# Kernel tuning notes

Hardware: AMD Instinct MI355X
Metric: run time of the kernel (lower is better)

## Reference

```python
import math
from collections import deque
import jax, jax.numpy as jnp
import numpy as np

PS = 16; DF = 256; DS = 16; DLANG = 896; BETA = 2.0
B_SZ = 2; IMG = 512


def setup_inputs():
    key = jax.random.key(0)
    ks = jax.random.split(key, 16)
    def rn(k, shape, scale=1.0):
        return jax.random.normal(k, shape, jnp.float32) * scale
    # W_delta bias init: inverse-softplus of dt ~ LogUniform(1e-3, 1e-1), as in torch _init_weights
    u = jax.random.uniform(ks[15], (DF,), jnp.float32)
    dt = jnp.exp(u * (math.log(0.1) - math.log(0.001)) + math.log(0.001))
    inv_dt = dt + jnp.log(-jnp.expm1(-dt))
    return {
        "images": rn(ks[0], (B_SZ, 3, IMG, IMG)),
        "lang_g": rn(ks[1], (B_SZ, DLANG)),
        "conv1_w": rn(ks[2], (64, 3, 3, 3), 1.0 / math.sqrt(27)),
        "conv1_b": jnp.zeros((64,), jnp.float32),
        "conv2_w": rn(ks[3], (128, 64, 3, 3), 1.0 / math.sqrt(576)),
        "conv2_b": jnp.zeros((128,), jnp.float32),
        "fc_w": rn(ks[4], (DF, 128), 1.0 / math.sqrt(128)),
        "fc_b": jnp.zeros((DF,), jnp.float32),
        "W_gate": rn(ks[5], (DF, DLANG), 1.0 / math.sqrt(DLANG)),
        "W_g_prime": rn(ks[6], (DF, DLANG), 1.0 / math.sqrt(DLANG)),
        "A_log": jnp.log(jnp.broadcast_to(jnp.arange(1, DS + 1, dtype=jnp.float32), (DF, DS))),
        "D": jnp.ones((DF,), jnp.float32),
        "B_w": rn(ks[7], (DS, DF), 1.0 / math.sqrt(DF)),
        "B_b": jnp.zeros((DS,), jnp.float32),
        "C_w": rn(ks[8], (DS, DF), 1.0 / math.sqrt(DF)),
        "C_b": jnp.zeros((DS,), jnp.float32),
        "Wd_w": rn(ks[9], (DF, DF), 1.0 / math.sqrt(DF)),
        "Wd_b": inv_dt,
        "out_w": rn(ks[10], (DF, DF), 1.0 / math.sqrt(DF)),
        "out_b": jnp.zeros((DF,), jnp.float32),
        "ln_g": jnp.ones((DF,), jnp.float32),
        "ln_b": jnp.zeros((DF,), jnp.float32),
    }


def _gelu(x):
    return jax.nn.gelu(x, approximate=False)  # torch nn.GELU() default = exact erf


def _conv(x, w, b):
    y = jax.lax.conv_general_dilated(x, w, (1, 1), 'SAME', dimension_numbers=('NCHW', 'OIHW', 'NCHW'))
    return y + b[None, :, None, None]


def _patch_feats(images, c1w, c1b, c2w, c2b, fcw, fcb):
    B, C, H, W = images.shape
    nH, nW = H // PS, W // PS
    # non-overlapping patchify (== unfold/unfold in torch)
    p = images.reshape(B, C, nH, PS, nW, PS).transpose(0, 2, 4, 1, 3, 5).reshape(B * nH * nW, C, PS, PS)
    h = _gelu(_conv(p, c1w, c1b))
    h = _gelu(_conv(h, c2w, c2b))
    h = h.mean(axis=(2, 3))  # AdaptiveAvgPool2d((1,1))
    feats = (h @ fcw.T + fcb).reshape(B, nH * nW, DF)
    return feats, nH, nW


def _structure(feats, r_sem, nH, nW):
    # Host-side (numpy) Kruskal MST + BFS ordering, mirroring the torch detach().cpu() path.
    f = np.asarray(feats, np.float32)
    r = np.asarray(r_sem, np.float32)
    B, P, _ = f.shape
    src, dst = [], []
    for i in range(nH):
        for j in range(nW):
            u = i * nW + j
            if j + 1 < nW:
                src.append(u); dst.append(u + 1)
            if i + 1 < nH:
                src.append(u); dst.append(u + nW)
    src = np.array(src); dst = np.array(dst)
    bfs_all, par_all = [], []
    for b in range(B):
        fn = f[b] / np.maximum(np.linalg.norm(f[b], axis=1, keepdims=True), 1e-12)
        cos = (fn[src] * fn[dst]).sum(1)
        w = (1.0 - r[b][src]) * (1.0 - r[b][dst]) * (-cos) + 1e-6
        parent = np.arange(P)
        def find(x):
            while parent[x] != x:
                parent[x] = parent[parent[x]]
                x = parent[x]
            return x
        adj = [[] for _ in range(P)]
        cnt = 0
        for idx in np.argsort(w):
            ru, rv = find(int(src[idx])), find(int(dst[idx]))
            if ru != rv:
                parent[ru] = rv
                adj[src[idx]].append(int(dst[idx]))
                adj[dst[idx]].append(int(src[idx]))
                cnt += 1
                if cnt == P - 1:
                    break
        root = int(r[b].argmax())
        vis = [False] * P; par_of = [-1] * P; bfs = []
        q = deque([root]); vis[root] = True
        while q:
            n = q.popleft()
            bfs.append(n)
            for nb in adj[n]:
                if not vis[nb]:
                    vis[nb] = True
                    par_of[nb] = n
                    q.append(nb)
        o2b = [0] * P
        for bi, oi in enumerate(bfs):
            o2b[oi] = bi
        par_bfs = [-1 if par_of[o] == -1 else o2b[par_of[o]] for o in bfs]
        bfs_all.append(bfs); par_all.append(par_bfs)
    return jnp.array(bfs_all, jnp.int32), jnp.array(par_all, jnp.int32)


def _core(feats, r_sem, g_prime, bfs, par, A_log, D, B_w, B_b, C_w, C_b, Wd_w, Wd_b, out_w, out_b, ln_g, ln_b):
    A = -jnp.exp(A_log)  # (DF, DS)
    def one(f_b, r_b, gp, bfs_b, par_b):
        rs = r_b[bfs_b]                                  # (P,)
        X = f_b[bfs_b] + rs[:, None] * gp[None, :]       # (P, DF)
        delta = jax.nn.softplus(X @ Wd_w.T + Wd_b) * (1.0 + BETA * rs[:, None])
        Bp = X @ B_w.T + B_b                             # (P, DS)
        Cp = X @ C_w.T + C_b                             # (P, DS)
        P = X.shape[0]
        def body(H, inp):
            i, d_i, b_i, c_i, x_i, p_i = inp
            A_bar = jnp.exp(d_i[:, None] * A)            # (DF, DS)
            h_par = H[jnp.maximum(p_i, 0)] * (p_i >= 0)  # zeros at root
            h = A_bar * h_par + (d_i[:, None] * b_i[None, :]) * x_i[:, None]
            H = H.at[i].set(h)
            y = (h * c_i[None, :]).sum(-1) + D * x_i
            return H, y
        H0 = jnp.zeros((P, DF, DS), X.dtype)
        _, Y = jax.lax.scan(body, H0, (jnp.arange(P), delta, Bp, Cp, X, par_b))
        Yr = jnp.zeros_like(Y).at[bfs_b].set(Y)          # scatter back to raster order
        o = Yr @ out_w.T + out_b
        mu = o.mean(-1, keepdims=True)
        v = ((o - mu) ** 2).mean(-1, keepdims=True)
        return ln_g * (o - mu) / jnp.sqrt(v + 1e-5) + ln_b
    return jax.vmap(one)(feats, r_sem, g_prime, bfs, par)


def reference(images, lang_g, conv1_w, conv1_b, conv2_w, conv2_b, fc_w, fc_b, W_gate, W_g_prime, A_log, D, B_w, B_b, C_w, C_b, Wd_w, Wd_b, out_w, out_b, ln_g, ln_b):
    feats, nH, nW = _patch_feats(images, conv1_w, conv1_b, conv2_w, conv2_b, fc_w, fc_b)
    g_proj = lang_g @ W_gate.T
    r_sem = jax.nn.sigmoid(jnp.einsum('bd,bpd->bp', g_proj, feats) / math.sqrt(DF))
    bfs, par = _structure(feats, r_sem, nH, nW)
    g_prime = lang_g @ W_g_prime.T
    return _core(feats, r_sem, g_prime, bfs, par, A_log, D, B_w, B_b, C_w, C_b, Wd_w, Wd_b, out_w, out_b, ln_g, ln_b)
```

## Files before the change

### kernel.cpp

```cpp
#include <hip/hip_runtime.h>
#include <cstddef>
#include <cstdint>

#define NB    2
#define NP    1024
#define DFEAT 256
#define DSTATE 16
#define NEDGE 1984

typedef unsigned short ushortb;

typedef float fx16 __attribute__((ext_vector_type(16)));
typedef short s16x8 __attribute__((ext_vector_type(8)));

__device__ __forceinline__ float bf2f(unsigned short u){
  union { unsigned int i; float f; } c; c.i = ((unsigned int)u) << 16; return c.f;
}
__device__ __forceinline__ unsigned short f2bf(float f){
  union { float f; unsigned int i; } c; c.f = f;
  unsigned int u = c.i;
  unsigned int r = (u + 0x7fffu + ((u >> 16) & 1u)) >> 16;
  return (unsigned short)r;
}
__device__ __forceinline__ float ldin(const void* p, size_t i, int isbf){
  return isbf ? bf2f(((const ushortb*)p)[i]) : ((const float*)p)[i];
}
__device__ __forceinline__ float gelu_f(float x){
  return 0.5f * x * (1.0f + erff(x * 0.70710678118654752f));
}
__device__ __forceinline__ unsigned int f2sort(float f){
  union { float f; unsigned int i; } c; c.f = f;
  return (c.i & 0x80000000u) ? ~c.i : (c.i | 0x80000000u);
}

constexpr size_t AL(size_t x){ return (x + 63) & ~(size_t)63; }
constexpr size_t O_W1    = 0;
constexpr size_t O_B1    = AL(O_W1 + 1728);
constexpr size_t O_W2    = AL(O_B1 + 64);
constexpr size_t O_B2    = AL(O_W2 + 73728);
constexpr size_t O_FCW   = AL(O_B2 + 128);
constexpr size_t O_FCB   = AL(O_FCW + 32768);
constexpr size_t O_WDW   = AL(O_FCB + 256);
constexpr size_t O_WDB   = AL(O_WDW + 65536);
constexpr size_t O_BWO   = AL(O_WDB + 256);
constexpr size_t O_BBO   = AL(O_BWO + 4096);
constexpr size_t O_CWO   = AL(O_BBO + 16);
constexpr size_t O_CBO   = AL(O_CWO + 4096);
constexpr size_t O_OW    = AL(O_CBO + 16);
constexpr size_t O_OB    = AL(O_OW + 65536);
constexpr size_t O_AF    = AL(O_OB + 256);
constexpr size_t O_DD    = AL(O_AF + 4096);
constexpr size_t O_LNG   = AL(O_DD + 256);
constexpr size_t O_LNB   = AL(O_LNG + 256);
constexpr size_t O_FEATS = AL(O_LNB + 256);
constexpr size_t O_GPROJ = AL(O_FEATS + (size_t)NB*NP*DFEAT);
constexpr size_t O_GPRIM = AL(O_GPROJ + NB*DFEAT);
constexpr size_t O_RSEM  = AL(O_GPRIM + NB*DFEAT);
constexpr size_t O_BFS   = AL(O_RSEM + NB*NP);
constexpr size_t O_PAR   = AL(O_BFS + NB*NP);
constexpr size_t O_X     = AL(O_PAR + NB*NP);
constexpr size_t O_DELTA = AL(O_X + (size_t)NB*NP*DFEAT);
constexpr size_t O_BP    = AL(O_DELTA + (size_t)NB*NP*DFEAT);
constexpr size_t O_CP    = AL(O_BP + NB*NP*DSTATE);
constexpr size_t O_YR    = AL(O_CP + NB*NP*DSTATE);
constexpr size_t O_FLAG  = AL(O_YR + (size_t)NB*NP*DFEAT);
constexpr size_t O_LVL   = AL(O_FLAG + 64);

__global__ __launch_bounds__(256) void k_sniff(const void* img, float* ws)
{
  __shared__ int cnt;
  int tid = threadIdx.x;
  if (tid == 0) cnt = 0;
  __syncthreads();
  const ushortb* u = (const ushortb*)img;
  int local = 0;
  for (int k = 0; k < 16; k++){
    unsigned short v = u[tid * 16 + k];
    if (v == 0 || v == 0x8000u){ local++; continue; }
    float f = fabsf(bf2f(v));
    if (f >= 1e-8f && f <= 64.f) local++;
  }
  atomicAdd(&cnt, local);
  __syncthreads();
  if (tid == 0) ((int*)(ws + O_FLAG))[0] = (cnt >= 3900) ? 1 : 0;
}

__global__ __launch_bounds__(256) void k_convert(const void* c1w, const void* c1b, const void* c2w,
                          const void* c2b, const void* fcw, const void* fcb,
                          const void* alog, const void* dvec,
                          const void* bw, const void* bb, const void* cw, const void* cb,
                          const void* wdw, const void* wdb,
                          const void* ow, const void* ob,
                          const void* lng, const void* lnb,
                          const void* lang, const void* wgate, const void* wgp,
                          float* ws)
{
  const int F = ((const int*)(ws + O_FLAG))[0];
  if (blockIdx.x >= 3038){
    int row = (blockIdx.x - 3038) * 4 + (threadIdx.x >> 6);
    int lane = threadIdx.x & 63;
    int mat = row >> 9;
    int b   = (row >> 8) & 1;
    int df  = row & 255;
    const void* W = mat ? wgp : wgate;
    float s = 0.f;
    for (int k = lane; k < 896; k += 64)
      s += ldin(lang, (size_t)b * 896 + k, F) * ldin(W, (size_t)df * 896 + k, F);
    s += __shfl_xor(s, 1);  s += __shfl_xor(s, 2);  s += __shfl_xor(s, 4);
    s += __shfl_xor(s, 8);  s += __shfl_xor(s, 16); s += __shfl_xor(s, 32);
    if (lane == 0) ws[(mat ? O_GPRIM : O_GPROJ) + b * 256 + df] = s;
    return;
  }
  if (blockIdx.x >= 990){
    size_t i2 = (size_t)(blockIdx.x - 990) * 256 + threadIdx.x;
    if (i2 < (size_t)NB * NP * DFEAT) ws[O_YR + i2] = 0.f;
    return;
  }
  int i = blockIdx.x * 256 + threadIdx.x;
  if (i < 1728){ ws[O_W1 + i] = ldin(c1w, i, F); return; } i -= 1728;
  if (i < 64){ ws[O_B1 + i] = ldin(c1b, i, F); return; } i -= 64;
  if (i < 73728){
    int sg = i >> 11;
    int r = i & 2047;
    int nt = r >> 9;
    int r2 = r & 511;
    int ln = r2 >> 3, e = r2 & 7;
    int c  = sg / 18, s = sg - c * 18;
    int tap = s >> 1, ksub = s & 1;
    int oc = nt * 32 + (ln & 31);
    int ic = c * 32 + ksub * 16 + (ln >> 5) * 8 + e;
    float v = ldin(c2w, (size_t)(oc * 64 + ic) * 9 + tap, F);
    ushortb hi = f2bf(v);
    float lo = v - bf2f(hi);
    ushortb* WB = (ushortb*)(ws + O_W2);
    size_t cb = ((size_t)(sg * 4 + nt)) * 2;
    WB[cb * 512 + r2]       = hi;
    WB[(cb + 1) * 512 + r2] = f2bf(lo);
    return;
  } i -= 73728;
  if (i < 128){ ws[O_B2 + i] = ldin(c2b, i, F); return; } i -= 128;
  if (i < 32768){ ws[O_FCW + i] = ldin(fcw, i, F); return; } i -= 32768;
  if (i < 256){ ws[O_FCB + i] = ldin(fcb, i, F); return; } i -= 256;
  if (i < 65536){
    int k = i >> 8, df = i & 255;
    ws[O_WDW + i] = ldin(wdw, (size_t)df * 256 + k, F); return;
  } i -= 65536;
  if (i < 256){ ws[O_WDB + i] = ldin(wdb, i, F); return; } i -= 256;
  if (i < 4096){
    int k = i >> 4, s = i & 15;
    ws[O_BWO + i] = ldin(bw, (size_t)s * 256 + k, F); return;
  } i -= 4096;
  if (i < 16){ ws[O_BBO + i] = ldin(bb, i, F); return; } i -= 16;
  if (i < 4096){
    int k = i >> 4, s = i & 15;
    ws[O_CWO + i] = ldin(cw, (size_t)s * 256 + k, F); return;
  } i -= 4096;
  if (i < 16){ ws[O_CBO + i] = ldin(cb, i, F); return; } i -= 16;
  if (i < 65536){
    int k = i >> 8, df = i & 255;
    ws[O_OW + i] = ldin(ow, (size_t)df * 256 + k, F); return;
  } i -= 65536;
  if (i < 256){ ws[O_OB + i] = ldin(ob, i, F); return; } i -= 256;
  if (i < 4096){ ws[O_AF + i] = -expf(ldin(alog, i, F)); return; } i -= 4096;
  if (i < 256){ ws[O_DD + i] = ldin(dvec, i, F); return; } i -= 256;
  if (i < 256){ ws[O_LNG + i] = ldin(lng, i, F); return; } i -= 256;
  if (i < 256){ ws[O_LNB + i] = ldin(lnb, i, F); }
}

__global__ __launch_bounds__(512, 4) void k_patch(const void* __restrict__ img,
                                                  const float* __restrict__ ws,
                                                  float* __restrict__ feats)
{
  __shared__ __align__(16) ushortb Abuf[2 * 10368];
  __shared__ float timg[768];
  __shared__ float pool4[512];
  __shared__ float pm[128];
  const int F = ((const int*)(ws + O_FLAG))[0];
  const float* W1 = ws + O_W1;  const float* B1 = ws + O_B1;
  const float* FCW = ws + O_FCW; const float* FCB = ws + O_FCB;
  const s16x8* BF = (const s16x8*)(ws + O_W2);

  int blk = blockIdx.x; int b = blk >> 10; int pidx = blk & 1023;
  int ph = pidx >> 5, pw = pidx & 31;
  int tid = threadIdx.x;

  if (tid < 256){
    int y = tid >> 4, x = tid & 15;
    #pragma unroll
    for (int c = 0; c < 3; c++)
      timg[c * 256 + tid] =
        ldin(img, (((size_t)b * 3 + c) * 512 + (ph * 16 + y)) * 512 + (pw * 16 + x), F);
  }
  {
    uint4 z4 = make_uint4(0u, 0u, 0u, 0u);
    for (int r = tid; r < 324; r += 512){
      int y = r / 18, x = r - y * 18;
      if (y == 0 || y == 17 || x == 0 || x == 17){
        #pragma unroll
        for (int m = 0; m < 4; m++){
          *(uint4*)&Abuf[r * 32 + m * 8] = z4;
          *(uint4*)&Abuf[10368 + r * 32 + m * 8] = z4;
        }
      }
    }
  }
  __syncthreads();

  int wv = tid >> 6, ln = tid & 63;
  int mg = wv >> 1, ng = wv & 1;
  int l31 = ln & 31, lhi = ln >> 5;
  int xcol = ln & 15, yrow = l31 >> 4;
  int p = tid & 255, og = tid >> 8;
  int ii = p >> 4, jj = p & 15;

  fx16 acc00, acc01, acc10, acc11;
  #pragma unroll
  for (int r = 0; r < 16; r++){ acc00[r] = 0.f; acc01[r] = 0.f; acc10[r] = 0.f; acc11[r] = 0.f; }

  for (int c = 0; c < 2; c++){
    {
      float pin[27];
      #pragma unroll
      for (int cc = 0; cc < 3; cc++)
        #pragma unroll
        for (int dy = 0; dy < 3; dy++)
          #pragma unroll
          for (int dx = 0; dx < 3; dx++){
            int y = ii + dy - 1, x = jj + dx - 1;
            bool ok = (y >= 0 && y < 16 && x >= 0 && x < 16);
            pin[cc * 9 + dy * 3 + dx] = ok ? timg[cc * 256 + y * 16 + x] : 0.f;
          }
      int oc0 = c * 32 + og * 16;
      int w1base = __builtin_amdgcn_readfirstlane(oc0 * 27);
      const float* W1g = W1 + w1base;
      int r = (ii + 1) * 18 + (jj + 1);
      int swz = ((r >> 1) & 3) << 3;
      #pragma unroll
      for (int g = 0; g < 2; g++){
        float av[8];
        #pragma unroll
        for (int o = 0; o < 8; o++){
          float a = B1[oc0 + g * 8 + o];
          #pragma unroll
          for (int t = 0; t < 27; t++) a += W1g[(g * 8 + o) * 27 + t] * pin[t];
          av[o] = gelu_f(a);
        }
        unsigned int hp[4], lp[4];
        #pragma unroll
        for (int q = 0; q < 4; q++){
          float v0 = av[2 * q], v1 = av[2 * q + 1];
          ushortb h0 = f2bf(v0), h1 = f2bf(v1);
          float l0 = v0 - bf2f(h0), l1 = v1 - bf2f(h1);
          hp[q] = (unsigned int)h0 | ((unsigned int)h1 << 16);
          lp[q] = (unsigned int)f2bf(l0) | ((unsigned int)f2bf(l1) << 16);
        }
        int idx = r * 32 + (((og * 2 + g) << 3) ^ swz);
        *(uint4*)&Abuf[idx] = make_uint4(hp[0], hp[1], hp[2], hp[3]);
        *(uint4*)&Abuf[10368 + idx] = make_uint4(lp[0], lp[1], lp[2], lp[3]);
      }
    }
    __syncthreads();

    {
      const s16x8* bfp = BF + (size_t)((c * 144 + ng * 4) * 64 + ln);
      for (int s = 0; s < 18; s++){
        int tap = s >> 1, ksub = s & 1;
        int dyq = tap / 3, dxq = tap - dyq * 3;
        int icq0 = (ksub << 1) + lhi;
        int rA = (mg * 4 + yrow + dyq) * 18 + (xcol + dxq);
        int rB = rA + 36;
        int iA0 = rA * 32 + ((icq0 ^ ((rA >> 1) & 3)) << 3);
        int iA1 = rB * 32 + ((icq0 ^ ((rB >> 1) & 3)) << 3);
        s16x8 fa0h = *(const s16x8*)&Abuf[iA0];
        s16x8 fa0l = *(const s16x8*)&Abuf[10368 + iA0];
        s16x8 fa1h = *(const s16x8*)&Abuf[iA1];
        s16x8 fa1l = *(const s16x8*)&Abuf[10368 + iA1];
        const s16x8* bq = bfp + (s << 9);
        s16x8 fb0h = bq[0];
        s16x8 fb0l = bq[64];
        s16x8 fb1h = bq[128];
        s16x8 fb1l = bq[192];
        acc00 = __builtin_amdgcn_mfma_f32_32x32x16_bf16(fa0h, fb0h, acc00, 0, 0, 0);
        acc01 = __builtin_amdgcn_mfma_f32_32x32x16_bf16(fa0h, fb1h, acc01, 0, 0, 0);
        acc10 = __builtin_amdgcn_mfma_f32_32x32x16_bf16(fa1h, fb0h, acc10, 0, 0, 0);
        acc11 = __builtin_amdgcn_mfma_f32_32x32x16_bf16(fa1h, fb1h, acc11, 0, 0, 0);
        acc00 = __builtin_amdgcn_mfma_f32_32x32x16_bf16(fa0l, fb0h, acc00, 0, 0, 0);
        acc01 = __builtin_amdgcn_mfma_f32_32x32x16_bf16(fa0l, fb1h, acc01, 0, 0, 0);
        acc10 = __builtin_amdgcn_mfma_f32_32x32x16_bf16(fa1l, fb0h, acc10, 0, 0, 0);
        acc11 = __builtin_amdgcn_mfma_f32_32x32x16_bf16(fa1l, fb1h, acc11, 0, 0, 0);
        acc00 = __builtin_amdgcn_mfma_f32_32x32x16_bf16(fa0h, fb0l, acc00, 0, 0, 0);
        acc01 = __builtin_amdgcn_mfma_f32_32x32x16_bf16(fa0h, fb1l, acc01, 0, 0, 0);
        acc10 = __builtin_amdgcn_mfma_f32_32x32x16_bf16(fa1h, fb0l, acc10, 0, 0, 0);
        acc11 = __builtin_amdgcn_mfma_f32_32x32x16_bf16(fa1h, fb1l, acc11, 0, 0, 0);
      }
    }
    __syncthreads();
  }

  #pragma unroll
  for (int n = 0; n < 2; n++){
    int nt = ng * 2 + n;
    float bz = ws[O_B2 + nt * 32 + l31];
    float sum = 0.f;
    #pragma unroll
    for (int r = 0; r < 16; r++)
      sum += gelu_f(((n == 0) ? acc00[r] : acc01[r]) + bz)
           + gelu_f(((n == 0) ? acc10[r] : acc11[r]) + bz);
    sum += __shfl_xor(sum, 32);
    if (lhi == 0) pool4[mg * 128 + nt * 32 + l31] = sum;
  }
  __syncthreads();
  if (tid < 128){
    float sv = pool4[tid] + pool4[128 + tid] + pool4[256 + tid] + pool4[384 + tid];
    pm[tid] = sv * (1.f / 256.f);
  }
  __syncthreads();

  if (tid < 256){
    int df = tid;
    float s = FCB[df];
    const float* wrow = FCW + (size_t)df * 128;
    #pragma unroll
    for (int k = 0; k < 128; k += 4)
      s += wrow[k] * pm[k] + wrow[k + 1] * pm[k + 1]
         + wrow[k + 2] * pm[k + 2] + wrow[k + 3] * pm[k + 3];
    feats[((size_t)(b * 1024 + pidx)) * 256 + df] = s;
  }
}

__device__ __forceinline__ void edge_uv(int e, int& u, int& v){
  if (e < 1953){
    int i = e / 63; int k = e - i * 63;
    if (k < 62){ int j = k >> 1; u = i * 32 + j; v = (k & 1) ? u + 32 : u + 1; }
    else { u = i * 32 + 31; v = u + 32; }
  } else { u = 31 * 32 + (e - 1953); v = u + 1; }
}

__global__ __launch_bounds__(1024) void k_struct(float* __restrict__ ws)
{
  __shared__ float s_ninv[1024];
  __shared__ float s_w[NEDGE];
  __shared__ float s_r[1024];
  __shared__ int   s_comp[1024];
  __shared__ int   s_link[1024];
  __shared__ int   s_link2[1024];
  __shared__ unsigned long long s_best[1024];
  __shared__ unsigned char  s_mst[NEDGE];
  __shared__ unsigned short s_adj[1024 * 4];
  __shared__ unsigned char  s_deg[1024];
  __shared__ unsigned short s_bfs[1024];
  __shared__ short          s_parof[1024];
  __shared__ unsigned short s_o2b[1024];
  __shared__ unsigned short s_cur[1024];
  __shared__ unsigned short s_nxt[1024];
  __shared__ unsigned short s_off[1025];
  __shared__ unsigned short s_loff2[1026];
  __shared__ unsigned long long s_rootkey;
  __shared__ int s_ncomp, s_cursz, s_bfscnt, s_nextsz, s_nlvl;

  int b = blockIdx.x; int tid = threadIdx.x;
  const float* feats = ws + O_FEATS + (size_t)b * NP * DFEAT;

  {
    const float4* f4 = (const float4*)(feats + (size_t)tid * 256);
    const float4* g4 = (const float4*)(ws + O_GPROJ + b * 256);
    float d = 0.f, gdot = 0.f;
    for (int k = 0; k < 64; k++){
      float4 q = f4[k]; float4 g = g4[k];
      d += q.x*q.x + q.y*q.y + q.z*q.z + q.w*q.w;
      gdot += q.x*g.x + q.y*g.y + q.z*g.z + q.w*g.w;
    }
    s_ninv[tid] = 1.f / fmaxf(sqrtf(d), 1e-12f);
    float r = 1.f / (1.f + expf(-gdot * (1.f / 16.f)));
    s_r[tid] = r;
    ws[O_RSEM + b * NP + tid] = r;
    s_comp[tid] = tid;
    s_deg[tid] = 0;
    s_bfs[tid] = (unsigned short)tid;
    s_o2b[tid] = (unsigned short)tid;
    s_parof[tid] = -1;
  }
  for (int e = tid; e < NEDGE; e += 1024) s_mst[e] = 0;
  __syncthreads();

  for (int e = tid; e < NEDGE; e += 1024){
    int u, v; edge_uv(e, u, v);
    const float4* fu = (const float4*)(feats + (size_t)u * 256);
    const float4* fv = (const float4*)(feats + (size_t)v * 256);
    float d = 0.f;
    for (int k = 0; k < 64; k++){ float4 a = fu[k], c = fv[k]; d += a.x*c.x + a.y*c.y + a.z*c.z + a.w*c.w; }
    float cosv = d * s_ninv[u] * s_ninv[v];
    s_w[e] = (1.f - s_r[u]) * (1.f - s_r[v]) * (-cosv) + 1e-6f;
  }
  __syncthreads();

  for (int round = 0; round < 12; round++){
    s_best[tid] = ~0ull;
    __syncthreads();
    for (int e = tid; e < NEDGE; e += 1024){
      int u, v; edge_uv(e, u, v);
      int cu = s_comp[u], cv = s_comp[v];
      if (cu != cv){
        unsigned long long key = (((unsigned long long)f2sort(s_w[e])) << 32) | (unsigned int)e;
        atomicMin(&s_best[cu], key);
        atomicMin(&s_best[cv], key);
      }
    }
    __syncthreads();
    int l = tid;
    if (s_comp[tid] == tid && s_best[tid] != ~0ull){
      int e = (int)(s_best[tid] & 0xffffffffu);
      int u, v; edge_uv(e, u, v);
      s_mst[e] = 1;
      int cu = s_comp[u], cv = s_comp[v];
      l = (cu == tid) ? cv : cu;
    }
    s_link[tid] = l;
    __syncthreads();
    if (l != tid && s_link[l] == tid && tid < l) s_link[tid] = tid;
    __syncthreads();
    {
      int x = tid;
      int p = s_link[x];
      while (p != x){ x = p; p = s_link[x]; }
      s_link2[tid] = x;
    }
    __syncthreads();
    s_comp[tid] = s_link2[s_comp[tid]];
    if (tid == 0) s_ncomp = 0;
    __syncthreads();
    if (s_comp[tid] == tid) atomicAdd(&s_ncomp, 1);
    __syncthreads();
    if (s_ncomp == 1) break;
    __syncthreads();
  }
  __syncthreads();

  {
    int v = tid; int i = v >> 5, j = v & 31;
    float wloc[4]; int nloc[4]; int d = 0;
    if (j > 0){ int e = (i < 31) ? (i * 63 + 2 * (j - 1)) : (1953 + (j - 1));
      if (s_mst[e]){ wloc[d] = s_w[e]; nloc[d] = v - 1; d++; } }
    if (j < 31){ int e = (i < 31) ? (i * 63 + 2 * j) : (1953 + j);
      if (s_mst[e]){ wloc[d] = s_w[e]; nloc[d] = v + 1; d++; } }
    if (i > 0){ int e = (i - 1) * 63 + ((j < 31) ? (2 * j + 1) : 62);
      if (s_mst[e]){ wloc[d] = s_w[e]; nloc[d] = v - 32; d++; } }
    if (i < 31){ int e = i * 63 + ((j < 31) ? (2 * j + 1) : 62);
      if (s_mst[e]){ wloc[d] = s_w[e]; nloc[d] = v + 32; d++; } }
    for (int a = 1; a < d; a++){
      float wv = wloc[a]; int nv = nloc[a]; int c = a - 1;
      while (c >= 0 && wloc[c] > wv){ wloc[c+1] = wloc[c]; nloc[c+1] = nloc[c]; c--; }
      wloc[c+1] = wv; nloc[c+1] = nv;
    }
    s_deg[v] = (unsigned char)d;
    for (int a = 0; a < d; a++) s_adj[v * 4 + a] = (unsigned short)nloc[a];
  }
  if (tid == 0) s_rootkey = 0ull;
  __syncthreads();
  {
    unsigned long long key = (((unsigned long long)f2sort(s_r[tid])) << 32) | (unsigned int)(1023 - tid);
    atomicMax(&s_rootkey, key);
  }
  __syncthreads();
  int root = 1023 - (int)(s_rootkey & 0xffffffffu);

  if (tid == 0){
    s_bfs[0] = (unsigned short)root; s_o2b[root] = 0; s_parof[root] = -1;
    s_cur[0] = (unsigned short)root; s_cursz = 1; s_bfscnt = 1; s_nlvl = 0;
  }
  __syncthreads();
  for (int lev = 0; lev < 1024; lev++){
    int csz = s_cursz;
    if (csz <= 0) break;
    if (tid < 64){
      int runbase = 0;
      for (int t0 = 0; t0 < csz; t0 += 64){
        int t = t0 + tid;
        int cnt = 0;
        if (t < csz){
          int n = s_cur[t];
          cnt = (int)s_deg[n] - (s_parof[n] >= 0 ? 1 : 0);
        }
        int v = cnt;
        #pragma unroll
        for (int off = 1; off < 64; off <<= 1){
          int u2 = __shfl_up(v, off);
          if (tid >= off) v += u2;
        }
        if (t < csz) s_off[t] = (unsigned short)(runbase + v - cnt);
        runbase += __shfl(v, 63);
      }
      if (tid == 0){
        if (s_nlvl < 1025){ s_loff2[s_nlvl] = (unsigned short)(s_bfscnt - csz); }
        s_nlvl++;
        s_nextsz = runbase;
      }
    }
    __syncthreads();
    if (tid < csz){
      int n = s_cur[tid]; int base = s_off[tid]; int k = 0;
      int pn = s_parof[n]; int dg = s_deg[n];
      for (int a = 0; a < dg; a++){
        int c = s_adj[n * 4 + a];
        if (c == pn) continue;
        s_parof[c] = (short)n;
        if (base + k < 1024) s_nxt[base + k] = (unsigned short)c;
        int pos = s_bfscnt + base + k;
        if (pos < 1024){
          s_bfs[pos] = (unsigned short)c;
          s_o2b[c] = (unsigned short)pos;
        }
        k++;
      }
    }
    __syncthreads();
    if (tid == 0){ s_bfscnt += s_nextsz; s_cursz = (s_nextsz > 1024) ? 1024 : s_nextsz; }
    __syncthreads();
    if (tid < s_cursz) s_cur[tid] = s_nxt[tid];
    __syncthreads();
  }
  __syncthreads();

  int* BFSo = (int*)(ws + O_BFS);
  int* PARo = (int*)(ws + O_PAR);
  {
    int node = s_bfs[tid] & 1023;
    BFSo[b * 1024 + tid] = node;
    int p = s_parof[node];
    PARo[b * 1024 + tid] = (p < 0) ? -1 : (int)(s_o2b[p] & 1023);
  }
  {
    int* LVLo = (int*)(ws + O_LVL) + b * 1040;
    int nl = s_nlvl; if (nl > 1024) nl = 1024;
    if (tid == 0){ LVLo[0] = nl; LVLo[1 + nl] = NP; }
    if (tid < nl) LVLo[1 + tid] = (int)s_loff2[tid];
  }
}

__global__ __launch_bounds__(256) void k_xdelta(float* __restrict__ ws)
{
  __shared__ float xs[256];
  int blk = blockIdx.x; int b = blk >> 10, i = blk & 1023; int df = threadIdx.x;
  const int* BFSo = (const int*)(ws + O_BFS);
  int node = BFSo[b * 1024 + i] & 1023;
  float rs = ws[O_RSEM + b * 1024 + node];
  float xv = ws[O_FEATS + ((size_t)(b * 1024 + node)) * 256 + df] + rs * ws[O_GPRIM + b * 256 + df];
  xs[df] = xv;
  ws[O_X + ((size_t)(b * 1024 + i)) * 256 + df] = xv;
  __syncthreads();
  {
    const float* WT = ws + O_WDW;
    float z = ws[O_WDB + df];
    #pragma unroll 8
    for (int k = 0; k < 256; k++)
      z += WT[(size_t)k * 256 + df] * xs[k];
    float sp = fmaxf(z, 0.f) + log1pf(expf(-fabsf(z)));
    ws[O_DELTA + ((size_t)(b * 1024 + i)) * 256 + df] = sp * (1.f + 2.f * rs);
  }
  if (df < 32){
    int s = df & 15;
    const float* WT = ws + ((df < 16) ? O_BWO : O_CWO);
    float a = ws[((df < 16) ? O_BBO : O_CBO) + s];
    #pragma unroll 8
    for (int k = 0; k < 256; k++) a += WT[k * 16 + s] * xs[k];
    ws[((df < 16) ? O_BP : O_CP) + (size_t)(b * 1024 + i) * 16 + s] = a;
  }
}

__global__ __launch_bounds__(256) void k_scan(float* __restrict__ ws)
{
  __shared__ float h[NP * DSTATE];
  __shared__ float xs[NP];
  __shared__ float ds[NP];
  __shared__ int   par_s[NP];
  __shared__ int   bfs_s[NP];
  int blk = blockIdx.x; int b = blk >> 8, f = blk & 255;
  int tid = threadIdx.x;
  int g = tid >> 4, s = tid & 15;
  const int* PARo = (const int*)(ws + O_PAR);
  const int* BFSo = (const int*)(ws + O_BFS);
  const int* LVLo = (const int*)(ws + O_LVL) + b * 1040;
  for (int i = tid; i < NP; i += 256){
    xs[i] = ws[O_X     + ((size_t)(b * NP + i)) * DFEAT + f];
    ds[i] = ws[O_DELTA + ((size_t)(b * NP + i)) * DFEAT + f];
    par_s[i] = PARo[b * NP + i];
    bfs_s[i] = BFSo[b * NP + i] & 1023;
  }
  __syncthreads();

  int nlvl = LVLo[0];
  bool degen = (nlvl < 1 || nlvl > NP);
  if (degen) nlvl = NP;

  float Aln = ws[O_AF + f * 16 + s];
  float Dv  = ws[O_DD + f];
  const float* Bp = ws + O_BP + (size_t)b * NP * DSTATE;
  const float* Cp = ws + O_CP + (size_t)b * NP * DSTATE;
  float* Yr = ws + O_YR + (size_t)b * NP * DFEAT;

  for (int l = 0; l < nlvl; l++){
    int o0, o1;
    if (degen){ o0 = l; o1 = l + 1; }
    else {
      o0 = LVLo[1 + l]; o1 = LVLo[2 + l];
      o0 = (o0 < 0) ? 0 : ((o0 > NP) ? NP : o0);
      o1 = (o1 < o0) ? o0 : ((o1 > NP) ? NP : o1);
    }
    for (int i = o0 + g; i < o1; i += 16){
      int p = par_s[i];
      float d = ds[i], x = xs[i];
      float hp = (p >= 0 && p < i) ? h[p * 16 + s] : 0.f;
      float hn = expf(d * Aln) * hp + d * Bp[i * 16 + s] * x;
      h[i * 16 + s] = hn;
      float t = hn * Cp[i * 16 + s];
      t += __shfl_xor(t, 1); t += __shfl_xor(t, 2);
      t += __shfl_xor(t, 4); t += __shfl_xor(t, 8);
      if (s == 0) Yr[(size_t)bfs_s[i] * DFEAT + f] = t + Dv * x;
    }
    __syncthreads();
  }
}

__global__ __launch_bounds__(256) void k_outln(const float* __restrict__ ws,
                                               void* __restrict__ out)
{
  __shared__ float yl[256];
  __shared__ float red[8];
  const int F = ((const int*)(ws + O_FLAG))[0];
  int blk = blockIdx.x; int b = blk >> 10, p = blk & 1023; int df = threadIdx.x;
  yl[df] = ws[O_YR + ((size_t)(b * 1024 + p)) * 256 + df];
  __syncthreads();
  const float* OT = ws + O_OW;
  float a = ws[O_OB + df];
  #pragma unroll 8
  for (int k = 0; k < 256; k++)
    a += OT[(size_t)k * 256 + df] * yl[k];
  int lane = df & 63, wid = df >> 6;
  float t = a;
  t += __shfl_xor(t, 1); t += __shfl_xor(t, 2);  t += __shfl_xor(t, 4);
  t += __shfl_xor(t, 8); t += __shfl_xor(t, 16); t += __shfl_xor(t, 32);
  if (lane == 0) red[wid] = t;
  __syncthreads();
  float mu = (red[0] + red[1] + red[2] + red[3]) * (1.f / 256.f);
  float dv = a - mu;
  float t2 = dv * dv;
  t2 += __shfl_xor(t2, 1); t2 += __shfl_xor(t2, 2);  t2 += __shfl_xor(t2, 4);
  t2 += __shfl_xor(t2, 8); t2 += __shfl_xor(t2, 16); t2 += __shfl_xor(t2, 32);
  if (lane == 0) red[4 + wid] = t2;
  __syncthreads();
  float var = (red[4] + red[5] + red[6] + red[7]) * (1.f / 256.f);
  float o = ws[O_LNG + df] * dv / sqrtf(var + 1e-5f) + ws[O_LNB + df];
  size_t idx = ((size_t)(b * 1024 + p)) * 256 + df;
  if (F) ((ushortb*)out)[idx] = f2bf(o);
  else   ((float*)out)[idx]   = o;
}

extern "C" void kernel_launch(void* const* d_in, const int* in_sizes, int n_in,
                              void* d_out, int out_size, void* d_ws, size_t ws_size,
                              hipStream_t stream)
{
  (void)in_sizes; (void)n_in; (void)out_size; (void)ws_size;
  const void* img   = d_in[0];
  const void* lang  = d_in[1];
  const void* c1w   = d_in[2];
  const void* c1b   = d_in[3];
  const void* c2w   = d_in[4];
  const void* c2b   = d_in[5];
  const void* fcw   = d_in[6];
  const void* fcb   = d_in[7];
  const void* wgate = d_in[8];
  const void* wgp   = d_in[9];
  const void* alog  = d_in[10];
  const void* dvec  = d_in[11];
  const void* bw    = d_in[12];
  const void* bb    = d_in[13];
  const void* cw    = d_in[14];
  const void* cb    = d_in[15];
  const void* wdw   = d_in[16];
  const void* wdb   = d_in[17];
  const void* ow    = d_in[18];
  const void* ob    = d_in[19];
  const void* lng   = d_in[20];
  const void* lnb   = d_in[21];
  float* ws = (float*)d_ws;

  k_sniff<<<1, 256, 0, stream>>>(img, ws);
  k_convert<<<990 + 2048 + 256, 256, 0, stream>>>(c1w, c1b, c2w, c2b, fcw, fcb, alog, dvec,
                                                  bw, bb, cw, cb, wdw, wdb, ow, ob, lng, lnb,
                                                  lang, wgate, wgp, ws);
  k_patch<<<2048, 512, 0, stream>>>(img, ws, ws + O_FEATS);
  k_struct<<<2, 1024, 0, stream>>>(ws);
  k_xdelta<<<2048, 256, 0, stream>>>(ws);
  k_scan<<<NB * DFEAT, 256, 0, stream>>>(ws);
  k_outln<<<2048, 256, 0, stream>>>(ws, d_out);
}
```

Before: 886.0 us.

## Stage both conv1 channel halves in LDS and split conv2 MFMA by row per wave

The conv1 output for both 32-channel halves is now computed once into a doubled LDS buffer, which removes the mid-loop barriers and the second pass. Conv2 tiling changes so that each of the 8 waves owns two output rows and loops over two output-channel passes with two accumulators, instead of a 2x4 mg/ng split with four accumulators. This cuts register pressure and barriers, but doubles the LDS footprint (about 83KB), which may lower occupancy, and each wave now reloads the B fragments for every pass.

```diff
diff --git a/kernel.cpp b/kernel.cpp
--- a/kernel.cpp
+++ b/kernel.cpp
@@ -171,9 +171,9 @@
                                                   const float* __restrict__ ws,
                                                   float* __restrict__ feats)
 {
-  __shared__ __align__(16) ushortb Abuf[2 * 10368];
+  __shared__ __align__(16) ushortb Abuf[4 * 10368];
   __shared__ float timg[768];
-  __shared__ float pool4[512];
+  __shared__ float pool8[8 * 128];
   __shared__ float pm[128];
   const int F = ((const int*)(ws + O_FLAG))[0];
   const float* W1 = ws + O_W1;  const float* B1 = ws + O_B1;
@@ -197,44 +197,39 @@
       int y = r / 18, x = r - y * 18;
       if (y == 0 || y == 17 || x == 0 || x == 17){
         #pragma unroll
-        for (int m = 0; m < 4; m++){
-          *(uint4*)&Abuf[r * 32 + m * 8] = z4;
-          *(uint4*)&Abuf[10368 + r * 32 + m * 8] = z4;
-        }
+        for (int pl = 0; pl < 4; pl++)
+          #pragma unroll
+          for (int m = 0; m < 4; m++)
+            *(uint4*)&Abuf[pl * 10368 + r * 32 + m * 8] = z4;
       }
     }
   }
   __syncthreads();
 
   int wv = tid >> 6, ln = tid & 63;
-  int mg = wv >> 1, ng = wv & 1;
   int l31 = ln & 31, lhi = ln >> 5;
   int xcol = ln & 15, yrow = l31 >> 4;
   int p = tid & 255, og = tid >> 8;
   int ii = p >> 4, jj = p & 15;
 
-  fx16 acc00, acc01, acc10, acc11;
-  #pragma unroll
-  for (int r = 0; r < 16; r++){ acc00[r] = 0.f; acc01[r] = 0.f; acc10[r] = 0.f; acc11[r] = 0.f; }
-
-  for (int c = 0; c < 2; c++){
-    {
-      float pin[27];
+  {
+    float pin[27];
+    #pragma unroll
+    for (int cc = 0; cc < 3; cc++)
       #pragma unroll
-      for (int cc = 0; cc < 3; cc++)
+      for (int dy = 0; dy < 3; dy++)
         #pragma unroll
-        for (int dy = 0; dy < 3; dy++)
-          #pragma unroll
-          for (int dx = 0; dx < 3; dx++){
-            int y = ii + dy - 1, x = jj + dx - 1;
-            bool ok = (y >= 0 && y < 16 && x >= 0 && x < 16);
-            pin[cc * 9 + dy * 3 + dx] = ok ? timg[cc * 256 + y * 16 + x] : 0.f;
-          }
+        for (int dx = 0; dx < 3; dx++){
+          int y = ii + dy - 1, x = jj + dx - 1;
+          bool ok = (y >= 0 && y < 16 && x >= 0 && x < 16);
+          pin[cc * 9 + dy * 3 + dx] = ok ? timg[cc * 256 + y * 16 + x] : 0.f;
+        }
+    int r = (ii + 1) * 18 + (jj + 1);
+    int swz = ((r >> 1) & 3) << 3;
+    for (int c = 0; c < 2; c++){
       int oc0 = c * 32 + og * 16;
       int w1base = __builtin_amdgcn_readfirstlane(oc0 * 27);
       const float* W1g = W1 + w1base;
-      int r = (ii + 1) * 18 + (jj + 1);
-      int swz = ((r >> 1) & 3) << 3;
       #pragma unroll
       for (int g = 0; g < 2; g++){
         float av[8];
@@ -255,63 +250,61 @@
           lp[q] = (unsigned int)f2bf(l0) | ((unsigned int)f2bf(l1) << 16);
         }
         int idx = r * 32 + (((og * 2 + g) << 3) ^ swz);
-        *(uint4*)&Abuf[idx] = make_uint4(hp[0], hp[1], hp[2], hp[3]);
-        *(uint4*)&Abuf[10368 + idx] = make_uint4(lp[0], lp[1], lp[2], lp[3]);
+        *(uint4*)&Abuf[c * 20736 + idx] = make_uint4(hp[0], hp[1], hp[2], hp[3]);
+        *(uint4*)&Abuf[c * 20736 + 10368 + idx] = make_uint4(lp[0], lp[1], lp[2], lp[3]);
       }
     }
-    __syncthreads();
-
-    {
-      const s16x8* bfp = BF + (size_t)((c * 144 + ng * 4) * 64 + ln);
+  }
+  __syncthreads();
+
+  #pragma unroll
+  for (int pass = 0; pass < 2; pass++){
+    fx16 acc0, acc1;
+    #pragma unroll
+    for (int r = 0; r < 16; r++){ acc0[r] = 0.f; acc1[r] = 0.f; }
+
+    for (int c = 0; c < 2; c++){
+      const ushortb* Ah = Abuf + c * 20736;
+      const s16x8* bfp = BF + (size_t)((c * 144 + pass * 4) * 64 + ln);
       for (int s = 0; s < 18; s++){
         int tap = s >> 1, ksub = s & 1;
         int dyq = tap / 3, dxq = tap - dyq * 3;
         int icq0 = (ksub << 1) + lhi;
-        int rA = (mg * 4 + yrow + dyq) * 18 + (xcol + dxq);
-        int rB = rA + 36;
-        int iA0 = rA * 32 + ((icq0 ^ ((rA >> 1) & 3)) << 3);
-        int iA1 = rB * 32 + ((icq0 ^ ((rB >> 1) & 3)) << 3);
-        s16x8 fa0h = *(const s16x8*)&Abuf[iA0];
-        s16x8 fa0l = *(const s16x8*)&Abuf[10368 + iA0];
-        s16x8 fa1h = *(const s16x8*)&Abuf[iA1];
-        s16x8 fa1l = *(const s16x8*)&Abuf[10368 + iA1];
+        int rA = (wv * 2 + yrow + dyq) * 18 + (xcol + dxq);
+        int iA = rA * 32 + ((icq0 ^ ((rA >> 1) & 3)) << 3);
+        s16x8 fa_h = *(const s16x8*)&Ah[iA];
+        s16x8 fa_l = *(const s16x8*)&Ah[10368 + iA];
         const s16x8* bq = bfp + (s << 9);
         s16x8 fb0h = bq[0];
         s16x8 fb0l = bq[64];
         s16x8 fb1h = bq[128];
         s16x8 fb1l = bq[192];
-        acc00 = __builtin_amdgcn_mfma_f32_32x32x16_bf16(fa0h, fb0h, acc00, 0, 0, 0);
-        acc01 = __builtin_amdgcn_mfma_f32_32x32x16_bf16(fa0h, fb1h, acc01, 0, 0, 0);
-        acc10 = __builtin_amdgcn_mfma_f32_32x32x16_bf16(fa1h, fb0h, acc10, 0, 0, 0);
-        acc11 = __builtin_amdgcn_mfma_f32_32x32x16_bf16(fa1h, fb1h, acc11, 0, 0, 0);
-        acc00 = __builtin_amdgcn_mfma_f32_32x32x16_bf16(fa0l, fb0h, acc00, 0, 0, 0);
-        acc01 = __builtin_amdgcn_mfma_f32_32x32x16_bf16(fa0l, fb1h, acc01, 0, 0, 0);
-        acc10 = __builtin_amdgcn_mfma_f32_32x32x16_bf16(fa1l, fb0h, acc10, 0, 0, 0);
-        acc11 = __builtin_amdgcn_mfma_f32_32x32x16_bf16(fa1l, fb1h, acc11, 0, 0, 0);
-        acc00 = __builtin_amdgcn_mfma_f32_32x32x16_bf16(fa0h, fb0l, acc00, 0, 0, 0);
-        acc01 = __builtin_amdgcn_mfma_f32_32x32x16_bf16(fa0h, fb1l, acc01, 0, 0, 0);
-        acc10 = __builtin_amdgcn_mfma_f32_32x32x16_bf16(fa1h, fb0l, acc10, 0, 0, 0);
-        acc11 = __builtin_amdgcn_mfma_f32_32x32x16_bf16(fa1h, fb1l, acc11, 0, 0, 0);
+        acc0 = __builtin_amdgcn_mfma_f32_32x32x16_bf16(fa_h, fb0h, acc0, 0, 0, 0);
+        acc1 = __builtin_amdgcn_mfma_f32_32x32x16_bf16(fa_h, fb1h, acc1, 0, 0, 0);
+        acc0 = __builtin_amdgcn_mfma_f32_32x32x16_bf16(fa_l, fb0h, acc0, 0, 0, 0);
+        acc1 = __builtin_amdgcn_mfma_f32_32x32x16_bf16(fa_l, fb1h, acc1, 0, 0, 0);
+        acc0 = __builtin_amdgcn_mfma_f32_32x32x16_bf16(fa_h, fb0l, acc0, 0, 0, 0);
+        acc1 = __builtin_amdgcn_mfma_f32_32x32x16_bf16(fa_h, fb1l, acc1, 0, 0, 0);
       }
     }
-    __syncthreads();
-  }
-
-  #pragma unroll
-  for (int n = 0; n < 2; n++){
-    int nt = ng * 2 + n;
-    float bz = ws[O_B2 + nt * 32 + l31];
-    float sum = 0.f;
+
     #pragma unroll
-    for (int r = 0; r < 16; r++)
-      sum += gelu_f(((n == 0) ? acc00[r] : acc01[r]) + bz)
-           + gelu_f(((n == 0) ? acc10[r] : acc11[r]) + bz);
-    sum += __shfl_xor(sum, 32);
-    if (lhi == 0) pool4[mg * 128 + nt * 32 + l31] = sum;
+    for (int n = 0; n < 2; n++){
+      int nt = pass * 2 + n;
+      float bz = ws[O_B2 + nt * 32 + l31];
+      float sum = 0.f;
+      #pragma unroll
+      for (int r = 0; r < 16; r++)
+        sum += gelu_f(((n == 0) ? acc0[r] : acc1[r]) + bz);
+      sum += __shfl_xor(sum, 32);
+      if (lhi == 0) pool8[wv * 128 + nt * 32 + l31] = sum;
+    }
   }
   __syncthreads();
   if (tid < 128){
-    float sv = pool4[tid] + pool4[128 + tid] + pool4[256 + tid] + pool4[384 + tid];
+    float sv = 0.f;
+    #pragma unroll
+    for (int w = 0; w < 8; w++) sv += pool8[w * 128 + tid];
     pm[tid] = sv * (1.f / 256.f);
   }
   __syncthreads();
```

New measurement: 868.6 us. 2.0% less time.
